# Kernel optimization log

Hardware: AMD Instinct MI355X
Metric: run time of the kernel (lower is better)

Reference implementation:

```python
import jax, jax.numpy as jnp
import numpy as np

EOS_IDX = 2
B, LAYERS, HEADS, SEQ = 1, 33, 20, 512


def setup_inputs() -> dict:
    key = jax.random.key(0)
    k1, k2, k3, k4 = jax.random.split(key, 4)
    tokens = jax.random.randint(k1, (B, SEQ), 0, 30)
    attentions = jax.random.normal(k2, (B, LAYERS, HEADS, SEQ, SEQ), dtype=jnp.float32)
    weight = jax.random.normal(k3, (LAYERS * HEADS,), dtype=jnp.float32) * 0.05
    bias = jax.random.normal(k4, (1,), dtype=jnp.float32) * 0.05
    return {"tokens": tokens, "attentions": attentions, "weight": weight, "bias": bias}


def reference(tokens, attentions, weight, bias):
    b, nl, nh, s, _ = attentions.shape
    # mask out positions at/after EOS token pairs
    eos = (tokens != EOS_IDX).astype(attentions.dtype)           # [B, S]
    mask2d = eos[:, None, :] * eos[:, :, None]                   # [B, S, S]
    att = attentions * mask2d[:, None, None, :, :]
    # [..., :-1, :-1] then [..., 1:, 1:] == drop first and last positions
    att = att[..., 1:-1, 1:-1]                                   # [B, L, H, S-2, S-2]
    att = att.reshape(b, nl * nh, s - 2, s - 2)                  # [B, F, s2, s2]
    # symmetrize
    sym = att + jnp.swapaxes(att, -1, -2)
    # average product correction
    a1 = sym.sum(-1, keepdims=True)                              # [B, F, s2, 1]
    a2 = sym.sum(-2, keepdims=True)                              # [B, F, 1, s2]
    a12 = sym.sum((-1, -2), keepdims=True)                       # [B, F, 1, 1]
    norm = sym - a1 * a2 / a12
    logits = jnp.einsum('bfij,f->bij', norm, weight) + bias[0]
    return jax.nn.sigmoid(logits)                                # [B, s2, s2]
```

## Files before the change

### kernel.cpp

```cpp
#include <hip/hip_runtime.h>
#include <math.h>

#define SEQ   512
#define NF    660
#define CROP  510
#define EOSI  2
#define RT    16
#define GH    20
#define NT_   32
#define NG    33

typedef float f4 __attribute__((ext_vector_type(4)));
typedef float f2 __attribute__((ext_vector_type(2)));

#define BARRIER_LGKM() asm volatile("s_waitcnt lgkmcnt(0)\n\ts_barrier" ::: "memory")

#define LOADP8(buf, f) do {                                                   \
    const float* _b = A + ((size_t)(f) << 18) + ((size_t)row0 << 9);          \
    buf[0] = *(const f4*)(_b + 4 * lane);                                     \
    buf[1] = *(const f4*)(_b + 256 + 4 * lane);                               \
    buf[2] = *(const f4*)(_b + 512 + 4 * lane);                               \
    buf[3] = *(const f4*)(_b + 768 + 4 * lane);                               \
    buf[4] = *(const f4*)(_b + 1024 + 4 * lane);                              \
    buf[5] = *(const f4*)(_b + 1280 + 4 * lane);                              \
    buf[6] = *(const f4*)(_b + 1536 + 4 * lane);                              \
    buf[7] = *(const f4*)(_b + 1792 + 4 * lane);                              \
} while (0)

#define COMP8(buf, wf, cacc, h) do {                                          \
    _Pragma("unroll")                                                         \
    for (int rr = 0; rr < 4; ++rr) {                                          \
        const float mi = mrow[rr];                                            \
        f4 x0 = buf[2 * rr], x1 = buf[2 * rr + 1];                            \
        float vals[8] = {x0[0], x0[1], x0[2], x0[3],                          \
                         x1[0], x1[1], x1[2], x1[3]};                         \
        float rs = 0.f;                                                       \
        _Pragma("unroll")                                                     \
        for (int e = 0; e < 8; ++e) {                                         \
            const float v = vals[e];                                          \
            wa_acc[rr][e] += (wf) * v;                                        \
            rs += mskv[e] * v;                                                \
            cacc[e] += mi * v;                                                \
        }                                                                     \
        _Pragma("unroll")                                                     \
        for (int off = 32; off > 0; off >>= 1)                                \
            rs += __shfl_down(rs, off, 64);                                   \
        if (lane == 0) rowstage[h][wave * 4 + rr] = rs;                       \
    }                                                                         \
} while (0)

#define FLUSHCOL(q) do {                                                      \
    float* __restrict__ _dst = colpart + ((size_t)t * NF + fbase + 4 * (q)) * SEQ; \
    const float* __restrict__ _src = &colstage[(q) & 1][0][0];                \
    *(f4*)(_dst + 4 * tid)        = *(const f4*)(_src + 4 * tid);             \
    *(f4*)(_dst + 1024 + 4 * tid) = *(const f4*)(_src + 1024 + 4 * tid);      \
} while (0)

#define COMBINE(cacc, h) do {                                                 \
    const int pp = (h) & 1;                                                   \
    _Pragma("unroll")                                                         \
    for (int e = 0; e < 8; ++e)                                               \
        col_lds[pp][wave][(e >> 2) * 256 + 4 * lane + (e & 3)] = cacc[e];     \
    BARRIER_LGKM();                                                           \
    if (((h) & 3) == 0 && (h) > 0) FLUSHCOL((h) / 4 - 1);                     \
    {                                                                         \
        const int c = 2 * tid;                                                \
        f2 s;                                                                 \
        s[0] = col_lds[pp][0][c]     + col_lds[pp][1][c]                      \
             + col_lds[pp][2][c]     + col_lds[pp][3][c];                     \
        s[1] = col_lds[pp][0][c + 1] + col_lds[pp][1][c + 1]                  \
             + col_lds[pp][2][c + 1] + col_lds[pp][3][c + 1];                 \
        *(f2*)&colstage[((h) >> 2) & 1][(h) & 3][c] = s;                      \
    }                                                                         \
} while (0)

__global__ __launch_bounds__(256, 3) void pass1_kernel(
    const float* __restrict__ A, const int* __restrict__ tokens,
    const float* __restrict__ weight,
    float* __restrict__ WApart, float* __restrict__ rowsum, float* __restrict__ colpart)
{
    __shared__ float msk[SEQ];
    __shared__ float col_lds[2][4][SEQ];
    __shared__ float colstage[2][4][SEQ];
    __shared__ float rowstage[GH][RT];

    const int t = blockIdx.x, g = blockIdx.y;
    const int tid = threadIdx.x, wave = tid >> 6, lane = tid & 63;
    const int fbase = g * GH;

    for (int j = tid; j < SEQ; j += 256)
        msk[j] = (j >= 1 && j <= SEQ - 2 && tokens[j] != EOSI) ? 1.f : 0.f;
    BARRIER_LGKM();

    float mskv[8];
    #pragma unroll
    for (int e = 0; e < 8; ++e)
        mskv[e] = msk[(e >> 2) * 256 + 4 * lane + (e & 3)];

    const int row0 = t * RT + wave * 4;
    const float mrow[4] = {msk[row0], msk[row0 + 1], msk[row0 + 2], msk[row0 + 3]};

    float wa_acc[4][8];
    #pragma unroll
    for (int r = 0; r < 4; ++r)
        #pragma unroll
        for (int e = 0; e < 8; ++e) wa_acc[r][e] = 0.f;

    f4 bufA[8], bufB[8];
    LOADP8(bufA, fbase);

    #pragma unroll 1
    for (int hh = 0; hh < 10; ++hh) {
        const int h0 = 2 * hh, h1 = h0 + 1;

        float cacc0[8] = {0, 0, 0, 0, 0, 0, 0, 0};
        LOADP8(bufB, fbase + h1);
        COMP8(bufA, weight[fbase + h0], cacc0, h0);
        COMBINE(cacc0, h0);

        float cacc1[8] = {0, 0, 0, 0, 0, 0, 0, 0};
        if (hh < 9) LOADP8(bufA, fbase + h0 + 2);
        COMP8(bufB, weight[fbase + h1], cacc1, h1);
        COMBINE(cacc1, h1);
    }

    BARRIER_LGKM();

    FLUSHCOL(4);

    #pragma unroll
    for (int it = 0; it < 2; ++it) {
        const int e = it * 256 + tid;
        if (e < GH * RT) {
            const int h = e >> 4, r = e & 15;
            rowsum[((size_t)(fbase + h) << 9) + t * RT + r] = rowstage[h][r];
        }
    }
    float* __restrict__ wp = WApart + (size_t)g * SEQ * SEQ;
    #pragma unroll
    for (int rr = 0; rr < 4; ++rr) {
        f4 o0 = {wa_acc[rr][0], wa_acc[rr][1], wa_acc[rr][2], wa_acc[rr][3]};
        f4 o1 = {wa_acc[rr][4], wa_acc[rr][5], wa_acc[rr][6], wa_acc[rr][7]};
        *(f4*)(wp + ((size_t)(row0 + rr) << 9) + 4 * lane) = o0;
        *(f4*)(wp + ((size_t)(row0 + rr) << 9) + 256 + 4 * lane) = o1;
    }
}

__global__ __launch_bounds__(512) void kernel2(
    const float* __restrict__ WApart, float* __restrict__ WA,
    const float* __restrict__ rowsum, const float* __restrict__ colpart,
    const int* __restrict__ tokens, const float* __restrict__ weight,
    float* __restrict__ a1, float* __restrict__ sfac)
{
    __shared__ float part[8];
    const int b = blockIdx.x, tid = threadIdx.x;
    if (b < 128) {
        const size_t idx4 = (size_t)b * 512 + tid;
        f4 a = *(const f4*)(WApart + 4 * idx4);
        #pragma unroll 8
        for (int g = 1; g < NG; ++g) {
            f4 x = *(const f4*)(WApart + (size_t)g * (SEQ * SEQ) + 4 * idx4);
            a += x;
        }
        *(f4*)(WA + 4 * idx4) = a;
    } else {
        const int f = b - 128, j = tid;
        float cs = 0.f;
        #pragma unroll 8
        for (int t = 0; t < NT_; ++t)
            cs += colpart[((size_t)t * NF + f) * SEQ + j];
        const float m = (j >= 1 && j <= SEQ - 2 && tokens[j] != EOSI) ? 1.f : 0.f;
        const float v = m * (rowsum[((size_t)f << 9) + j] + cs);
        a1[((size_t)f << 9) + j] = v;
        float s = v;
        #pragma unroll
        for (int off = 32; off > 0; off >>= 1)
            s += __shfl_down(s, off, 64);
        const int wave = tid >> 6, lane = tid & 63;
        if (lane == 0) part[wave] = s;
        __syncthreads();
        if (tid == 0) {
            float a12 = 0.f;
            #pragma unroll
            for (int k = 0; k < 8; ++k) a12 += part[k];
            sfac[f] = weight[f] / a12;
        }
    }
}

__global__ __launch_bounds__(256) void pass3_kernel(
    const float* __restrict__ WA, const float* __restrict__ a1,
    const float* __restrict__ sfac, const int* __restrict__ tokens,
    const float* __restrict__ bias, float* __restrict__ out)
{
    const int TI = blockIdx.y * 16;
    const int TJ = blockIdx.x * 16;
    const int tid = threadIdx.x;
    const int tx = tid & 15, ty = tid >> 4;

    __shared__ float u_s[32][17];
    __shared__ float v_s[32][17];

    float acc = 0.f;

    for (int f0 = 0; f0 < NF; f0 += 32) {
        #pragma unroll
        for (int c = 0; c < 4; ++c) {
            const int e = c * 256 + tid;
            const int arr = e >> 9, ff = (e >> 4) & 31, ii = e & 15;
            const int f = f0 + ff;
            float val = 0.f;
            if (f < NF) {
                if (arr == 0) {
                    int Iu = TI + 1 + ii; if (Iu > SEQ - 1) Iu = SEQ - 1;
                    val = a1[((size_t)f << 9) + Iu] * sfac[f];
                } else {
                    int Ju = TJ + 1 + ii; if (Ju > SEQ - 1) Ju = SEQ - 1;
                    val = a1[((size_t)f << 9) + Ju];
                }
            }
            if (arr == 0) u_s[ff][ii] = val; else v_s[ff][ii] = val;
        }
        __syncthreads();
        #pragma unroll
        for (int ff = 0; ff < 32; ++ff)
            acc += u_s[ff][ty] * v_s[ff][tx];
        __syncthreads();
    }

    const int i = TI + ty, j = TJ + tx;
    if (i < CROP && j < CROP) {
        const int I = i + 1, J = j + 1;
        const float mi = (tokens[I] != EOSI) ? 1.f : 0.f;
        const float mj = (tokens[J] != EOSI) ? 1.f : 0.f;
        const float first = mi * mj * (WA[((size_t)I << 9) + J] + WA[((size_t)J << 9) + I]);
        const float logit = first - acc + bias[0];
        out[(size_t)i * CROP + j] = 1.f / (1.f + expf(-logit));
    }
}

extern "C" void kernel_launch(void* const* d_in, const int* in_sizes, int n_in,
                              void* d_out, int out_size, void* d_ws, size_t ws_size,
                              hipStream_t stream) {
    const int*   tokens = (const int*)d_in[0];
    const float* A      = (const float*)d_in[1];
    const float* weight = (const float*)d_in[2];
    const float* bias   = (const float*)d_in[3];
    float* out = (float*)d_out;

    float* WApart  = (float*)d_ws;
    float* colpart = WApart + (size_t)NG * SEQ * SEQ;
    float* WA      = colpart + (size_t)NT_ * NF * SEQ;
    float* rowsum  = WA + (size_t)SEQ * SEQ;
    float* a1      = rowsum + (size_t)NF * SEQ;
    float* sfac    = a1 + (size_t)NF * SEQ;

    dim3 g1(NT_, NG);
    pass1_kernel<<<g1, 256, 0, stream>>>(A, tokens, weight, WApart, rowsum, colpart);

    kernel2<<<128 + NF, 512, 0, stream>>>(WApart, WA, rowsum, colpart, tokens, weight, a1, sfac);

    dim3 g3(32, 32);
    pass3_kernel<<<g3, 256, 0, stream>>>(WA, a1, sfac, tokens, bias, out);
}
```

Before: 227.0 us.

## Replace per-head LDS column reduction and barriers with LDS atomics into full staging

The per-head cross-wave column-sum reduction, which went through double-buffered LDS scratch with a barrier per head and periodic flushes, is replaced by LDS atomicAdd into a colstage buffer sized for all 20 heads. That buffer is zeroed up front and written to global memory once at the end. This removes 20 barriers from the main loop so the waves can run independently and overlap loads with compute. In exchange there are 4-way contended LDS float atomics, and LDS grows to about 40KB per block. The launch-bounds occupancy hint of 3 blocks is also dropped, which may change register allocation.

```diff
diff --git a/kernel.cpp b/kernel.cpp
--- a/kernel.cpp
+++ b/kernel.cpp
@@ -27,7 +27,8 @@
     buf[7] = *(const f4*)(_b + 1792 + 4 * lane);                              \
 } while (0)
 
-#define COMP8(buf, wf, cacc, h) do {                                          \
+#define COMP8A(buf, wf, h) do {                                               \
+    float cacc[8] = {0, 0, 0, 0, 0, 0, 0, 0};                                 \
     _Pragma("unroll")                                                         \
     for (int rr = 0; rr < 4; ++rr) {                                          \
         const float mi = mrow[rr];                                            \
@@ -47,41 +48,18 @@
             rs += __shfl_down(rs, off, 64);                                   \
         if (lane == 0) rowstage[h][wave * 4 + rr] = rs;                       \
     }                                                                         \
-} while (0)
-
-#define FLUSHCOL(q) do {                                                      \
-    float* __restrict__ _dst = colpart + ((size_t)t * NF + fbase + 4 * (q)) * SEQ; \
-    const float* __restrict__ _src = &colstage[(q) & 1][0][0];                \
-    *(f4*)(_dst + 4 * tid)        = *(const f4*)(_src + 4 * tid);             \
-    *(f4*)(_dst + 1024 + 4 * tid) = *(const f4*)(_src + 1024 + 4 * tid);      \
-} while (0)
-
-#define COMBINE(cacc, h) do {                                                 \
-    const int pp = (h) & 1;                                                   \
     _Pragma("unroll")                                                         \
     for (int e = 0; e < 8; ++e)                                               \
-        col_lds[pp][wave][(e >> 2) * 256 + 4 * lane + (e & 3)] = cacc[e];     \
-    BARRIER_LGKM();                                                           \
-    if (((h) & 3) == 0 && (h) > 0) FLUSHCOL((h) / 4 - 1);                     \
-    {                                                                         \
-        const int c = 2 * tid;                                                \
-        f2 s;                                                                 \
-        s[0] = col_lds[pp][0][c]     + col_lds[pp][1][c]                      \
-             + col_lds[pp][2][c]     + col_lds[pp][3][c];                     \
-        s[1] = col_lds[pp][0][c + 1] + col_lds[pp][1][c + 1]                  \
-             + col_lds[pp][2][c + 1] + col_lds[pp][3][c + 1];                 \
-        *(f2*)&colstage[((h) >> 2) & 1][(h) & 3][c] = s;                      \
-    }                                                                         \
+        atomicAdd(&colstage[h][(e >> 2) * 256 + 4 * lane + (e & 3)], cacc[e]); \
 } while (0)
 
-__global__ __launch_bounds__(256, 3) void pass1_kernel(
+__global__ __launch_bounds__(256) void pass1_kernel(
     const float* __restrict__ A, const int* __restrict__ tokens,
     const float* __restrict__ weight,
     float* __restrict__ WApart, float* __restrict__ rowsum, float* __restrict__ colpart)
 {
     __shared__ float msk[SEQ];
-    __shared__ float col_lds[2][4][SEQ];
-    __shared__ float colstage[2][4][SEQ];
+    __shared__ float colstage[GH][SEQ];
     __shared__ float rowstage[GH][RT];
 
     const int t = blockIdx.x, g = blockIdx.y;
@@ -90,7 +68,13 @@
 
     for (int j = tid; j < SEQ; j += 256)
         msk[j] = (j >= 1 && j <= SEQ - 2 && tokens[j] != EOSI) ? 1.f : 0.f;
-    BARRIER_LGKM();
+    {
+        f4* cz = (f4*)&colstage[0][0];
+        #pragma unroll
+        for (int it = 0; it < 10; ++it)
+            cz[it * 256 + tid] = (f4){0.f, 0.f, 0.f, 0.f};
+    }
+    __syncthreads();
 
     float mskv[8];
     #pragma unroll
@@ -112,22 +96,23 @@
     #pragma unroll 1
     for (int hh = 0; hh < 10; ++hh) {
         const int h0 = 2 * hh, h1 = h0 + 1;
-
-        float cacc0[8] = {0, 0, 0, 0, 0, 0, 0, 0};
         LOADP8(bufB, fbase + h1);
-        COMP8(bufA, weight[fbase + h0], cacc0, h0);
-        COMBINE(cacc0, h0);
-
-        float cacc1[8] = {0, 0, 0, 0, 0, 0, 0, 0};
+        COMP8A(bufA, weight[fbase + h0], h0);
         if (hh < 9) LOADP8(bufA, fbase + h0 + 2);
-        COMP8(bufB, weight[fbase + h1], cacc1, h1);
-        COMBINE(cacc1, h1);
+        COMP8A(bufB, weight[fbase + h1], h1);
     }
 
     BARRIER_LGKM();
 
-    FLUSHCOL(4);
-
+    {
+        float* __restrict__ dst = colpart + ((size_t)t * NF + fbase) * SEQ;
+        const float* __restrict__ src = &colstage[0][0];
+        #pragma unroll
+        for (int it = 0; it < 10; ++it) {
+            const int fl = (it * 256 + tid) * 4;
+            *(f4*)(dst + fl) = *(const f4*)(src + fl);
+        }
+    }
     #pragma unroll
     for (int it = 0; it < 2; ++it) {
         const int e = it * 256 + tid;
```

After: 358.6 us. +58.0%, slower.
